# Optimization experiments

Measured on AMD Instinct MI355X. Metric: run time of the kernel, lower is better.

Reference implementation:

```python
import jax, jax.numpy as jnp
import numpy as np

N_NODES = 100000
N_EDGES = 1600000
D_IN = 128
D_HID = 64
N_CLASSES = 64


def setup_inputs() -> dict:
    key = jax.random.key(0)
    ks = jax.random.split(key, 12)
    x = jax.random.normal(ks[0], (N_NODES, D_IN), dtype=jnp.float32)
    edge_index = jax.random.randint(ks[1], (2, N_EDGES), 0, N_NODES, dtype=jnp.int64)
    def lin(k, fan_in, fan_out):
        k1, k2 = jax.random.split(k)
        bound = 1.0 / np.sqrt(fan_in)
        w = jax.random.uniform(k1, (fan_in, fan_out), jnp.float32, -bound, bound)
        b = jax.random.uniform(k2, (fan_out,), jnp.float32, -bound, bound)
        return w, b
    w1a, b1a = lin(ks[2], D_IN, D_HID)
    w1b, b1b = lin(ks[3], D_HID, D_HID)
    w2a, b2a = lin(ks[4], D_HID, D_HID)
    w2b, b2b = lin(ks[5], D_HID, N_CLASSES)
    return {"x": x, "edge_index": edge_index,
            "w1a": w1a, "b1a": b1a, "w1b": w1b, "b1b": b1b,
            "w2a": w2a, "b2a": b2a, "w2b": w2b, "b2b": b2b}


def _gin_agg(x, src, dst):
    # GINConv with eps=0: (1+eps)*x_i + sum_{j->i} x_j
    agg = jax.ops.segment_sum(x[src], dst, num_segments=N_NODES)
    return x + agg


def reference(x, edge_index, w1a, b1a, w1b, b1b, w2a, b2a, w2b, b2b):
    src, dst = edge_index[0], edge_index[1]
    # conv1: MLP = Linear -> ReLU -> Linear -> ReLU
    h = _gin_agg(x, src, dst)
    h = jax.nn.relu(h @ w1a + b1a)
    h = jax.nn.relu(h @ w1b + b1b)
    # conv2: MLP = Linear -> ReLU -> Linear
    h = _gin_agg(h, src, dst)
    h = jax.nn.relu(h @ w2a + b2a)
    h = h @ w2b + b2b
    # global add pool over the single graph -> [1, num_classes]
    return jnp.sum(h, axis=0, keepdims=True)
```

## Files before the change

kernel.cpp:

```cpp
#include <hip/hip_runtime.h>

#define N_NODES 100000
#define N_EDGES 1600000
#define D_IN 128
#define D 64

#define NBLK 1000
#define EPB  1600
#define NB2  391
#define SC_M  (NB2 * NBLK)
#define SC_CH 1024
#define SC_NB ((SC_M + SC_CH - 1) / SC_CH)

__device__ __forceinline__ float bf2f(unsigned short u) {
    union { unsigned int i; float f; } q; q.i = ((unsigned int)u) << 16; return q.f;
}
__device__ __forceinline__ unsigned short f2bf(float f) {
    unsigned int u = __float_as_uint(f);
    unsigned int r = (u + 0x7FFFu + ((u >> 16) & 1u)) >> 16;
    return (unsigned short)r;
}
__device__ __forceinline__ void acc4(float4& a, ushort4 v) {
    a.x += bf2f(v.x); a.y += bf2f(v.y); a.z += bf2f(v.z); a.w += bf2f(v.w);
}


__global__ __launch_bounds__(256) void k_hist1(const int* __restrict__ dst,
                                               int* __restrict__ bh) {
    __shared__ int h[NB2];
    int t = threadIdx.x;
    for (int i = t; i < NB2; i += 256) h[i] = 0;
    __syncthreads();
    int base = blockIdx.x * EPB;
    for (int i = t; i < EPB; i += 256) atomicAdd(&h[dst[base + i] >> 8], 1);
    __syncthreads();
    for (int i = t; i < NB2; i += 256) bh[i * NBLK + blockIdx.x] = h[i];
}

__global__ __launch_bounds__(256) void k_scanA(const int* __restrict__ bh,
                                               int* __restrict__ part) {
    __shared__ int s[256];
    int t = threadIdx.x;
    int base = blockIdx.x * SC_CH + t * 4;
    int sum = 0;
    if (base + 3 < SC_M) {
        int4 v = *(const int4*)(bh + base);
        sum = (v.x + v.y) + (v.z + v.w);
    } else {
        for (int k = 0; k < 4; k++) if (base + k < SC_M) sum += bh[base + k];
    }
    s[t] = sum;
    __syncthreads();
    for (int o = 128; o > 0; o >>= 1) {
        if (t < o) s[t] += s[t + o];
        __syncthreads();
    }
    if (t == 0) part[blockIdx.x] = s[0];
}

__global__ __launch_bounds__(512) void k_scanB(int* __restrict__ part) {
    __shared__ int s[512];
    int t = threadIdx.x;
    int v = (t < SC_NB) ? part[t] : 0;
    s[t] = v;
    __syncthreads();
    for (int o = 1; o < 512; o <<= 1) {
        int x = (t >= o) ? s[t - o] : 0;
        __syncthreads();
        s[t] += x;
        __syncthreads();
    }
    if (t < SC_NB) part[t] = s[t] - v;
}

__global__ __launch_bounds__(256) void k_scanC(int* __restrict__ bh,
                                               const int* __restrict__ part) {
    __shared__ int s[256];
    int t = threadIdx.x;
    int base = blockIdx.x * SC_CH + t * 4;
    int4 v = {0, 0, 0, 0};
    if (base + 3 < SC_M) v = *(const int4*)(bh + base);
    else { for (int k = 0; k < 4; k++) if (base + k < SC_M) (&v.x)[k] = bh[base + k]; }
    int sum = (v.x + v.y) + (v.z + v.w);
    s[t] = sum;
    __syncthreads();
    for (int o = 1; o < 256; o <<= 1) {
        int x = (t >= o) ? s[t - o] : 0;
        __syncthreads();
        s[t] += x;
        __syncthreads();
    }
    int run = part[blockIdx.x] + s[t] - sum;
    int4 w;
    w.x = run; run += v.x;
    w.y = run; run += v.y;
    w.z = run; run += v.z;
    w.w = run;
    if (base + 3 < SC_M) *(int4*)(bh + base) = w;
    else { for (int k = 0; k < 4; k++) if (base + k < SC_M) bh[base + k] = (&w.x)[k]; }
}

__global__ __launch_bounds__(256) void k_scatter1(const int* __restrict__ src,
                                                  const int* __restrict__ dst,
                                                  const int* __restrict__ bh,
                                                  uint2* __restrict__ tmp) {
    __shared__ int cur[NB2];
    int t = threadIdx.x;
    for (int i = t; i < NB2; i += 256) cur[i] = bh[i * NBLK + blockIdx.x];
    __syncthreads();
    int base = blockIdx.x * EPB;
    for (int i = t; i < EPB; i += 256) {
        int d = dst[base + i];
        int sv = src[base + i];
        int p = atomicAdd(&cur[d >> 8], 1);
        tmp[p] = make_uint2((unsigned)d, (unsigned)sv);
    }
}

__global__ __launch_bounds__(256) void k_padsum(const uint2* __restrict__ tmp,
                                                const int* __restrict__ bh,
                                                int* __restrict__ degarr,
                                                int* __restrict__ pb) {
    __shared__ int deg[256];
    __shared__ int s[256];
    int b = blockIdx.x, t = threadIdx.x;
    int e0 = bh[b * NBLK];
    int e1 = (b == NB2 - 1) ? N_EDGES : bh[(b + 1) * NBLK];
    deg[t] = 0;
    __syncthreads();
    for (int i = e0 + t; i < e1; i += 256) atomicAdd(&deg[tmp[i].x & 255u], 1);
    __syncthreads();
    int node = b * 256 + t;
    int d = (node < N_NODES) ? deg[t] : 0;
    if (node < N_NODES) degarr[node] = d;
    int dp = (d + 7) & ~7;
    s[t] = dp;
    __syncthreads();
    for (int o = 128; o > 0; o >>= 1) {
        if (t < o) s[t] += s[t + o];
        __syncthreads();
    }
    if (t == 0) pb[b] = s[0];
}

__global__ __launch_bounds__(512) void k_scanP(int* __restrict__ pb) {
    __shared__ int s[512];
    int t = threadIdx.x;
    int v = (t < NB2) ? pb[t] : 0;
    s[t] = v;
    __syncthreads();
    for (int o = 1; o < 512; o <<= 1) {
        int x = (t >= o) ? s[t - o] : 0;
        __syncthreads();
        s[t] += x;
        __syncthreads();
    }
    if (t < NB2) pb[t] = s[t] - v;
}

__global__ __launch_bounds__(256) void k_build2(const uint2* __restrict__ tmp,
                                                const int* __restrict__ bh,
                                                const int* __restrict__ degarr,
                                                const int* __restrict__ pb,
                                                int* __restrict__ offs,
                                                int* __restrict__ csr) {
    __shared__ int s[256];
    __shared__ int startp[256];
    __shared__ int cur[256];
    int b = blockIdx.x, t = threadIdx.x;
    int e0 = bh[b * NBLK];
    int e1 = (b == NB2 - 1) ? N_EDGES : bh[(b + 1) * NBLK];
    int node = b * 256 + t;
    int d = (node < N_NODES) ? degarr[node] : 0;
    int dp = (d + 7) & ~7;
    s[t] = dp;
    __syncthreads();
    for (int o = 1; o < 256; o <<= 1) {
        int x = (t >= o) ? s[t - o] : 0;
        __syncthreads();
        s[t] += x;
        __syncthreads();
    }
    int st = pb[b] + s[t] - dp;
    startp[t] = st;
    cur[t] = st;
    if (node < N_NODES) {
        offs[node] = st;
        if (node == N_NODES - 1) offs[N_NODES] = st + dp;
    }
    __syncthreads();
    for (int i = e0 + t; i < e1; i += 256) {
        uint2 p = tmp[i];
        int pos = atomicAdd(&cur[p.x & 255u], 1);
        csr[pos] = (int)p.y;
    }
    __syncthreads();
    int end = startp[t] + dp;
    for (int p = cur[t]; p < end; p++) csr[p] = N_NODES;
}

__global__ __launch_bounds__(256) void k_gemm1(const float* __restrict__ x,
                                               const float* __restrict__ w,
                                               unsigned short* __restrict__ z) {
    __shared__ float ws[D_IN][D];
    __shared__ float xs[16][D_IN + 1];
    int t = threadIdx.x;
    {
        const float4* w4 = (const float4*)w;
        float4* s4 = (float4*)&ws[0][0];
        for (int i = t; i < (D_IN * D) / 4; i += 256) s4[i] = w4[i];
    }
    int r = t >> 4, c = t & 15;
    __syncthreads();
    for (int base = blockIdx.x * 16; base < N_NODES; base += gridDim.x * 16) {
        for (int i = t; i < 16 * (D_IN / 4); i += 256) {
            int row = i >> 5, k4 = i & 31;
            float4 v = ((const float4*)(x + (size_t)(base + row) * D_IN))[k4];
            xs[row][k4 * 4 + 0] = v.x; xs[row][k4 * 4 + 1] = v.y;
            xs[row][k4 * 4 + 2] = v.z; xs[row][k4 * 4 + 3] = v.w;
        }
        __syncthreads();
        float4 acc = {0.f, 0.f, 0.f, 0.f};
        for (int k = 0; k < D_IN; k++) {
            float xv = xs[r][k];
            float4 wv = *(const float4*)&ws[k][c * 4];
            acc.x += xv * wv.x; acc.y += xv * wv.y;
            acc.z += xv * wv.z; acc.w += xv * wv.w;
        }
        ushort4 p;
        p.x = f2bf(acc.x); p.y = f2bf(acc.y); p.z = f2bf(acc.z); p.w = f2bf(acc.w);
        *(ushort4*)(z + (size_t)(base + r) * D + c * 4) = p;
        __syncthreads();
    }
}

__device__ __forceinline__ void gather8u(float4& acc, const unsigned short* __restrict__ zz,
                                         const int* __restrict__ csr,
                                         int e0, int e1, size_t c4) {
    for (int e = e0; e < e1; e += 8) {
        int4 ia = *(const int4*)(csr + e);
        int4 ib = *(const int4*)(csr + e + 4);
        ushort4 v0 = *(const ushort4*)(zz + (size_t)ia.x * D + c4);
        ushort4 v1 = *(const ushort4*)(zz + (size_t)ia.y * D + c4);
        ushort4 v2 = *(const ushort4*)(zz + (size_t)ia.z * D + c4);
        ushort4 v3 = *(const ushort4*)(zz + (size_t)ia.w * D + c4);
        ushort4 v4 = *(const ushort4*)(zz + (size_t)ib.x * D + c4);
        ushort4 v5 = *(const ushort4*)(zz + (size_t)ib.y * D + c4);
        ushort4 v6 = *(const ushort4*)(zz + (size_t)ib.z * D + c4);
        ushort4 v7 = *(const ushort4*)(zz + (size_t)ib.w * D + c4);
        acc4(acc, v0); acc4(acc, v1); acc4(acc, v2); acc4(acc, v3);
        acc4(acc, v4); acc4(acc, v5); acc4(acc, v6); acc4(acc, v7);
    }
}

__global__ __launch_bounds__(256, 6) void k_conv1(const unsigned short* __restrict__ z,
                                                  const int* __restrict__ offs,
                                                  const int* __restrict__ csr,
                                                  const float* __restrict__ b1a,
                                                  const float* __restrict__ w1b,
                                                  const float* __restrict__ b1b,
                                                  const float* __restrict__ w2a,
                                                  unsigned short* __restrict__ u) {
    __shared__ unsigned short w1s[D][D];
    __shared__ unsigned short w2s[D][D];
    __shared__ float h1s[16][D + 1];
    __shared__ float h2s[16][D + 1];
    int t = threadIdx.x;
    int r = t >> 4, c = t & 15;
    {
        for (int i = t; i < (D * D) / 4; i += 256) {
            float4 a = ((const float4*)w1b)[i];
            ushort4 p; p.x = f2bf(a.x); p.y = f2bf(a.y); p.z = f2bf(a.z); p.w = f2bf(a.w);
            *(ushort4*)&(&w1s[0][0])[i * 4] = p;
            float4 b = ((const float4*)w2a)[i];
            ushort4 q; q.x = f2bf(b.x); q.y = f2bf(b.y); q.z = f2bf(b.z); q.w = f2bf(b.w);
            *(ushort4*)&(&w2s[0][0])[i * 4] = q;
        }
    }
    float4 vb1a = ((const float4*)b1a)[c];
    float4 vb1b = ((const float4*)b1b)[c];
    __syncthreads();

    const size_t c4 = (size_t)(c * 4);
    for (int base = blockIdx.x * 16; base < N_NODES; base += gridDim.x * 16) {
        int node = base + r;
        float4 acc = {vb1a.x, vb1a.y, vb1a.z, vb1a.w};
        acc4(acc, *(const ushort4*)(z + (size_t)node * D + c4));
        int e0 = offs[node], e1 = offs[node + 1];
        gather8u(acc, z, csr, e0, e1, c4);
        h1s[r][c * 4 + 0] = fmaxf(acc.x, 0.f);
        h1s[r][c * 4 + 1] = fmaxf(acc.y, 0.f);
        h1s[r][c * 4 + 2] = fmaxf(acc.z, 0.f);
        h1s[r][c * 4 + 3] = fmaxf(acc.w, 0.f);
        __syncthreads();
        float4 a2 = vb1b;
        for (int k = 0; k < D; k++) {
            float hv = h1s[r][k];
            ushort4 wv = *(const ushort4*)&w1s[k][c * 4];
            a2.x += hv * bf2f(wv.x); a2.y += hv * bf2f(wv.y);
            a2.z += hv * bf2f(wv.z); a2.w += hv * bf2f(wv.w);
        }
        h2s[r][c * 4 + 0] = fmaxf(a2.x, 0.f);
        h2s[r][c * 4 + 1] = fmaxf(a2.y, 0.f);
        h2s[r][c * 4 + 2] = fmaxf(a2.z, 0.f);
        h2s[r][c * 4 + 3] = fmaxf(a2.w, 0.f);
        __syncthreads();
        float4 a3 = {0.f, 0.f, 0.f, 0.f};
        for (int k = 0; k < D; k++) {
            float hv = h2s[r][k];
            ushort4 wv = *(const ushort4*)&w2s[k][c * 4];
            a3.x += hv * bf2f(wv.x); a3.y += hv * bf2f(wv.y);
            a3.z += hv * bf2f(wv.z); a3.w += hv * bf2f(wv.w);
        }
        ushort4 p;
        p.x = f2bf(a3.x); p.y = f2bf(a3.y); p.z = f2bf(a3.z); p.w = f2bf(a3.w);
        *(ushort4*)(u + (size_t)node * D + c4) = p;
        __syncthreads();
    }
}

__global__ __launch_bounds__(256) void k_conv2(const unsigned short* __restrict__ u,
                                               const int* __restrict__ offs,
                                               const int* __restrict__ csr,
                                               const float* __restrict__ b2a,
                                               float* __restrict__ colsum) {
    __shared__ float red[16][D + 1];
    int t = threadIdx.x;
    int r = t >> 4, c = t & 15;
    float4 vb = ((const float4*)b2a)[c];
    float4 cs = {0.f, 0.f, 0.f, 0.f};
    const size_t c4 = (size_t)(c * 4);
    for (int base = blockIdx.x * 16; base < N_NODES; base += gridDim.x * 16) {
        int node = base + r;
        float4 acc = {vb.x, vb.y, vb.z, vb.w};
        acc4(acc, *(const ushort4*)(u + (size_t)node * D + c4));
        int e0 = offs[node], e1 = offs[node + 1];
        gather8u(acc, u, csr, e0, e1, c4);
        cs.x += fmaxf(acc.x, 0.f); cs.y += fmaxf(acc.y, 0.f);
        cs.z += fmaxf(acc.z, 0.f); cs.w += fmaxf(acc.w, 0.f);
    }
    red[r][c * 4 + 0] = cs.x; red[r][c * 4 + 1] = cs.y;
    red[r][c * 4 + 2] = cs.z; red[r][c * 4 + 3] = cs.w;
    __syncthreads();
    if (r == 0) {
        float4 tot = {0.f, 0.f, 0.f, 0.f};
        for (int rr = 0; rr < 16; rr++) {
            tot.x += red[rr][c * 4 + 0]; tot.y += red[rr][c * 4 + 1];
            tot.z += red[rr][c * 4 + 2]; tot.w += red[rr][c * 4 + 3];
        }
        atomicAdd(&colsum[c * 4 + 0], tot.x);
        atomicAdd(&colsum[c * 4 + 1], tot.y);
        atomicAdd(&colsum[c * 4 + 2], tot.z);
        atomicAdd(&colsum[c * 4 + 3], tot.w);
    }
}

__global__ void k_final(const float* __restrict__ colsum, const float* __restrict__ w2b,
                        const float* __restrict__ b2b, float* __restrict__ out) {
    int j = threadIdx.x;
    float acc = (float)N_NODES * b2b[j];
    for (int k = 0; k < D; k++) acc += colsum[k] * w2b[k * D + j];
    out[j] = acc;
}


extern "C" void kernel_launch(void* const* d_in, const int* in_sizes, int n_in,
                              void* d_out, int out_size, void* d_ws, size_t ws_size,
                              hipStream_t stream) {
    const float* x   = (const float*)d_in[0];
    const int*   ei  = (const int*)d_in[1];
    const float* w1a = (const float*)d_in[2];
    const float* b1a = (const float*)d_in[3];
    const float* w1b = (const float*)d_in[4];
    const float* b1b = (const float*)d_in[5];
    const float* w2a = (const float*)d_in[6];
    const float* b2a = (const float*)d_in[7];
    const float* w2b = (const float*)d_in[8];
    const float* b2b = (const float*)d_in[9];
    float* out = (float*)d_out;

    const int* srcp = ei;
    const int* dstp = ei + N_EDGES;

    char* ws = (char*)d_ws;
    unsigned short* z = (unsigned short*)(ws + 0);
    unsigned short* u = (unsigned short*)(ws + 12800256);
    uint2* tmp    = (uint2*)(ws + 25600512);
    int*   csr    = (int*)(ws + 38400512);
    int*   bh     = (int*)(ws + 51200512);
    int*   degarr = (int*)(ws + 52764512);
    int*   offs   = (int*)(ws + 53164896);
    int*   pb     = (int*)(ws + 53564960);
    int*   part   = (int*)(ws + 53567008);
    float* colsum = (float*)(ws + 53569056);

    hipMemsetAsync(colsum, 0, D * sizeof(float), stream);
    hipMemsetAsync(z + (size_t)N_NODES * D, 0, D * sizeof(unsigned short), stream);
    hipMemsetAsync(u + (size_t)N_NODES * D, 0, D * sizeof(unsigned short), stream);

    k_hist1   <<<NBLK, 256, 0, stream>>>(dstp, bh);
    k_scanA   <<<SC_NB, 256, 0, stream>>>(bh, part);
    k_scanB   <<<1, 512, 0, stream>>>(part);
    k_scanC   <<<SC_NB, 256, 0, stream>>>(bh, part);
    k_scatter1<<<NBLK, 256, 0, stream>>>(srcp, dstp, bh, tmp);
    k_padsum  <<<NB2, 256, 0, stream>>>(tmp, bh, degarr, pb);
    k_scanP   <<<1, 512, 0, stream>>>(pb);
    k_build2  <<<NB2, 256, 0, stream>>>(tmp, bh, degarr, pb, offs, csr);

    k_gemm1<<<2048, 256, 0, stream>>>(x, w1a, z);
    k_conv1<<<2048, 256, 0, stream>>>(z, offs, csr, b1a, w1b, b1b, w2a, u);
    k_conv2<<<2048, 256, 0, stream>>>(u, offs, csr, b2a, colsum);
    k_final<<<1, 64, 0, stream>>>(colsum, w2b, b2b, out);
}
```

Baseline: 486.4 us.

## Split conv1 gather from its MLP so the gather kernel runs at higher occupancy

Splits the fused conv1 kernel into a gather-only aggregation kernel, which writes the bf16 ReLU output to a workspace buffer, and a separate dense MLP kernel. The gather kernels now use 8-wave launch bounds, no shared memory and one 16-node tile per block (6250 blocks), so more waves can keep memory latency hidden. The cost is an extra round trip of a 100000x64 bf16 intermediate through memory and one more launch. It also adds a bf16 rounding of h1 and reuses the tmp region for h1, relaying out the workspace offsets.

```diff
diff --git a/kernel.cpp b/kernel.cpp
--- a/kernel.cpp
+++ b/kernel.cpp
@@ -253,14 +253,33 @@
     }
 }
 
-__global__ __launch_bounds__(256, 6) void k_conv1(const unsigned short* __restrict__ z,
-                                                  const int* __restrict__ offs,
-                                                  const int* __restrict__ csr,
-                                                  const float* __restrict__ b1a,
-                                                  const float* __restrict__ w1b,
-                                                  const float* __restrict__ b1b,
-                                                  const float* __restrict__ w2a,
-                                                  unsigned short* __restrict__ u) {
+__global__ __launch_bounds__(256, 8) void k_agg1(const unsigned short* __restrict__ z,
+                                                 const int* __restrict__ offs,
+                                                 const int* __restrict__ csr,
+                                                 const float* __restrict__ b1a,
+                                                 unsigned short* __restrict__ h1) {
+    int t = threadIdx.x;
+    int r = t >> 4, c = t & 15;
+    float4 vb = ((const float4*)b1a)[c];
+    const size_t c4 = (size_t)(c * 4);
+    for (int base = blockIdx.x * 16; base < N_NODES; base += gridDim.x * 16) {
+        int node = base + r;
+        float4 acc = {vb.x, vb.y, vb.z, vb.w};
+        acc4(acc, *(const ushort4*)(z + (size_t)node * D + c4));
+        int e0 = offs[node], e1 = offs[node + 1];
+        gather8u(acc, z, csr, e0, e1, c4);
+        ushort4 p;
+        p.x = f2bf(fmaxf(acc.x, 0.f)); p.y = f2bf(fmaxf(acc.y, 0.f));
+        p.z = f2bf(fmaxf(acc.z, 0.f)); p.w = f2bf(fmaxf(acc.w, 0.f));
+        *(ushort4*)(h1 + (size_t)node * D + c4) = p;
+    }
+}
+
+__global__ __launch_bounds__(256) void k_mlp1(const unsigned short* __restrict__ h1,
+                                              const float* __restrict__ w1b,
+                                              const float* __restrict__ b1b,
+                                              const float* __restrict__ w2a,
+                                              unsigned short* __restrict__ u) {
     __shared__ unsigned short w1s[D][D];
     __shared__ unsigned short w2s[D][D];
     __shared__ float h1s[16][D + 1];
@@ -277,21 +296,17 @@
             *(ushort4*)&(&w2s[0][0])[i * 4] = q;
         }
     }
-    float4 vb1a = ((const float4*)b1a)[c];
     float4 vb1b = ((const float4*)b1b)[c];
     __syncthreads();
 
     const size_t c4 = (size_t)(c * 4);
     for (int base = blockIdx.x * 16; base < N_NODES; base += gridDim.x * 16) {
         int node = base + r;
-        float4 acc = {vb1a.x, vb1a.y, vb1a.z, vb1a.w};
-        acc4(acc, *(const ushort4*)(z + (size_t)node * D + c4));
-        int e0 = offs[node], e1 = offs[node + 1];
-        gather8u(acc, z, csr, e0, e1, c4);
-        h1s[r][c * 4 + 0] = fmaxf(acc.x, 0.f);
-        h1s[r][c * 4 + 1] = fmaxf(acc.y, 0.f);
-        h1s[r][c * 4 + 2] = fmaxf(acc.z, 0.f);
-        h1s[r][c * 4 + 3] = fmaxf(acc.w, 0.f);
+        ushort4 hv4 = *(const ushort4*)(h1 + (size_t)node * D + c4);
+        h1s[r][c * 4 + 0] = bf2f(hv4.x);
+        h1s[r][c * 4 + 1] = bf2f(hv4.y);
+        h1s[r][c * 4 + 2] = bf2f(hv4.z);
+        h1s[r][c * 4 + 3] = bf2f(hv4.w);
         __syncthreads();
         float4 a2 = vb1b;
         for (int k = 0; k < D; k++) {
@@ -319,11 +334,11 @@
     }
 }
 
-__global__ __launch_bounds__(256) void k_conv2(const unsigned short* __restrict__ u,
-                                               const int* __restrict__ offs,
-                                               const int* __restrict__ csr,
-                                               const float* __restrict__ b2a,
-                                               float* __restrict__ colsum) {
+__global__ __launch_bounds__(256, 8) void k_conv2(const unsigned short* __restrict__ u,
+                                                  const int* __restrict__ offs,
+                                                  const int* __restrict__ csr,
+                                                  const float* __restrict__ b2a,
+                                                  float* __restrict__ colsum) {
     __shared__ float red[16][D + 1];
     int t = threadIdx.x;
     int r = t >> 4, c = t & 15;
@@ -383,16 +398,17 @@
     const int* dstp = ei + N_EDGES;
 
     char* ws = (char*)d_ws;
-    unsigned short* z = (unsigned short*)(ws + 0);
-    unsigned short* u = (unsigned short*)(ws + 12800256);
-    uint2* tmp    = (uint2*)(ws + 25600512);
-    int*   csr    = (int*)(ws + 38400512);
-    int*   bh     = (int*)(ws + 51200512);
-    int*   degarr = (int*)(ws + 52764512);
-    int*   offs   = (int*)(ws + 53164896);
-    int*   pb     = (int*)(ws + 53564960);
-    int*   part   = (int*)(ws + 53567008);
-    float* colsum = (float*)(ws + 53569056);
+    unsigned short* z  = (unsigned short*)(ws + 0);
+    unsigned short* u  = (unsigned short*)(ws + 12800256);
+    uint2*          tmp = (uint2*)(ws + 25600512);
+    unsigned short* h1  = (unsigned short*)(ws + 25600512);
+    int*   csr    = (int*)(ws + 38400768);
+    int*   bh     = (int*)(ws + 48000000);
+    int*   degarr = (int*)(ws + 49564160);
+    int*   offs   = (int*)(ws + 49964160);
+    int*   pb     = (int*)(ws + 50364416);
+    int*   part   = (int*)(ws + 50366464);
+    float* colsum = (float*)(ws + 50368512);
 
     hipMemsetAsync(colsum, 0, D * sizeof(float), stream);
     hipMemsetAsync(z + (size_t)N_NODES * D, 0, D * sizeof(unsigned short), stream);
@@ -408,7 +424,8 @@
     k_build2  <<<NB2, 256, 0, stream>>>(tmp, bh, degarr, pb, offs, csr);
 
     k_gemm1<<<2048, 256, 0, stream>>>(x, w1a, z);
-    k_conv1<<<2048, 256, 0, stream>>>(z, offs, csr, b1a, w1b, b1b, w2a, u);
-    k_conv2<<<2048, 256, 0, stream>>>(u, offs, csr, b2a, colsum);
+    k_agg1 <<<6250, 256, 0, stream>>>(z, offs, csr, b1a, h1);
+    k_mlp1 <<<2048, 256, 0, stream>>>(h1, w1b, b1b, w2a, u);
+    k_conv2<<<6250, 256, 0, stream>>>(u, offs, csr, b2a, colsum);
     k_final<<<1, 64, 0, stream>>>(colsum, w2b, b2b, out);
 }
```

Result: slower. 895.7 us (+84.1%).
